# Kernel tuning notes

Hardware: AMD Instinct MI355X
Metric: run time of the kernel (lower is better)

Reference implementation:

```python
import jax, jax.numpy as jnp
import numpy as np

H = 16  # n_heads

def setup_inputs() -> dict:
    key = jax.random.key(0)
    ks = jax.random.split(key, 12)
    B, L, S, D = 4, 2048, 2048, 1024
    E = D // H  # d_keys = d_values = 64
    s = 1.0 / np.sqrt(D)
    inp = {
        "queries": jax.random.normal(ks[0], (B, L, D), jnp.float32),
        "keys": jax.random.normal(ks[1], (B, S, D), jnp.float32),
        "values": jax.random.normal(ks[2], (B, S, D), jnp.float32),
        # causal boolean mask: True = masked out
        "attn_mask": jnp.triu(jnp.ones((L, S), jnp.bool_), k=1)[None, None],
        "Wq": jax.random.normal(ks[3], (H * E, D), jnp.float32) * s,
        "bq": jnp.zeros((H * E,), jnp.float32),
        "Wk": jax.random.normal(ks[4], (H * E, D), jnp.float32) * s,
        "bk": jnp.zeros((H * E,), jnp.float32),
        "Wv": jax.random.normal(ks[5], (H * E, D), jnp.float32) * s,
        "bv": jnp.zeros((H * E,), jnp.float32),
        "Wo": jax.random.normal(ks[6], (D, H * E), jnp.float32) * s,
        "bo": jnp.zeros((D,), jnp.float32),
    }
    return inp


def reference(queries, keys, values, attn_mask, Wq, bq, Wk, bk, Wv, bv, Wo, bo):
    B, L, D = queries.shape
    S = keys.shape[1]
    E = Wq.shape[0] // H
    # QKV projections + head split: (B, L/S, H, E)
    q = (queries @ Wq.T + bq).reshape(B, L, H, E)
    k = (keys @ Wk.T + bk).reshape(B, S, H, E)
    v = (values @ Wv.T + bv).reshape(B, S, H, E)
    scale = 1.0 / jnp.sqrt(jnp.asarray(E, q.dtype))
    scores = jnp.einsum("blhe,bshe->bhls", q, k) * scale  # (B,H,L,S)
    scores = jnp.where(attn_mask, jnp.asarray(-jnp.inf, scores.dtype), scores)
    A = jax.nn.softmax(scores, axis=-1)
    out = jnp.einsum("bhls,bshe->blhe", A, v).reshape(B, L, H * E)
    return out @ Wo.T + bo
```

## Files before the change

kernel.cpp:

```cpp
#include <hip/hip_runtime.h>
#include <hip/hip_bf16.h>

typedef float f32x4 __attribute__((ext_vector_type(4)));
typedef short s16x8 __attribute__((ext_vector_type(8)));
typedef short s16x4 __attribute__((ext_vector_type(4)));
typedef unsigned short u16;

#define H_ 16
#define E_ 64
#define D_ 1024
#define L_ 2048
#define NQT 32
#define SCL2E 0.18033688011f

__device__ __forceinline__ u16 f2bf(float f) {
  union { float f; unsigned u; } v; v.f = f;
  unsigned u = v.u;
  u += 0x7fffu + ((u >> 16) & 1u);
  return (u16)(u >> 16);
}

__device__ __forceinline__ unsigned pkbf(float a, float b) {
  unsigned r;
  asm("v_cvt_pk_bf16_f32 %0, %1, %2" : "=v"(r) : "v"(a), "v"(b));
  return r;
}

__device__ __forceinline__ void gld16(const u16* g, u16* l) {
  __builtin_amdgcn_global_load_lds((const __attribute__((address_space(1))) void*)g,
                                   (__attribute__((address_space(3))) void*)l, 16, 0, 0);
}

__global__ __launch_bounds__(256) void cvtall(const float* __restrict__ q,
                                              const float* __restrict__ k,
                                              const float* __restrict__ v,
                                              const float* __restrict__ w0,
                                              const float* __restrict__ w1,
                                              const float* __restrict__ w2,
                                              const float* __restrict__ w3,
                                              u16* __restrict__ qd,
                                              u16* __restrict__ kd,
                                              u16* __restrict__ vd,
                                              u16* __restrict__ d0,
                                              u16* __restrict__ d1,
                                              u16* __restrict__ d2,
                                              u16* __restrict__ d3) {
  const int b = blockIdx.x;
  const float* src; u16* dst; float s = 1.0f; size_t off;
  if (b < 12288) {
    const int y = b >> 12, bx = b & 4095;
    src = y == 0 ? q : (y == 1 ? k : v);
    dst = y == 0 ? qd : (y == 1 ? kd : vd);
    off = ((size_t)bx * 256 + threadIdx.x) * 8;
  } else {
    const int b2 = b - 12288, y = b2 >> 9, bx = b2 & 511;
    src = y == 0 ? w0 : (y == 1 ? w1 : (y == 2 ? w2 : w3));
    dst = y == 0 ? d0 : (y == 1 ? d1 : (y == 2 ? d2 : d3));
    if (y == 0) s = SCL2E;
    off = ((size_t)bx * 256 + threadIdx.x) * 8;
  }
  const f32x4 a = *(const f32x4*)(src + off);
  const f32x4 c = *(const f32x4*)(src + off + 4);
  s16x8 r;
#pragma unroll
  for (int j = 0; j < 4; ++j) { r[j] = (short)f2bf(a[j] * s); r[j + 4] = (short)f2bf(c[j] * s); }
  *(s16x8*)(dst + off) = r;
}

template<int PERMUTE>
__global__ __launch_bounds__(256) void gemm_lds(const u16* __restrict__ A,
                                                const u16* __restrict__ W,
                                                const float* __restrict__ bias,
                                                void* __restrict__ outp,
                                                int M, int N, int K, float bsc)
{
  __shared__ __align__(16) u16 As[2][128][64];
  __shared__ __align__(16) u16 Bs[2][128][64];
  const int tid = threadIdx.x;
  const int m0 = blockIdx.y * 128, n0 = blockIdx.x * 128;
  const int w = tid >> 6, lane = tid & 63, g = lane >> 4, li = lane & 15;
  const int wr = w >> 1, wc = w & 1;

  int sOff[4];
#pragma unroll
  for (int j = 0; j < 4; ++j) {
    const int s = (w * 4 + j) * 64 + lane;
    const int row = s >> 3, c8 = s & 7;
    sOff[j] = row * K + ((c8 ^ (row & 7)) * 8);
  }

  f32x4 acc[4][4];
#pragma unroll
  for (int i = 0; i < 4; ++i)
#pragma unroll
    for (int j = 0; j < 4; ++j) acc[i][j] = (f32x4){0.f, 0.f, 0.f, 0.f};

  const u16* Abase = A + (size_t)m0 * K;
  const u16* Wbase = W + (size_t)n0 * K;
  const int swz = li & 7;

  auto STAGE = [&](int k0, int bf) {
#pragma unroll
    for (int j = 0; j < 4; ++j) {
      gld16(Abase + k0 + sOff[j], &As[bf][(w * 4 + j) * 8][0]);
      gld16(Wbase + k0 + sOff[j], &Bs[bf][(w * 4 + j) * 8][0]);
    }
  };

  STAGE(0, 0);
  __syncthreads();
  int buf = 0;
  for (int k0 = 0; k0 < K; k0 += 64) {
    if (k0 + 64 < K) STAGE(k0 + 64, buf ^ 1);

    s16x8 a[2][4], b[2][4];
#pragma unroll
    for (int kk = 0; kk < 2; ++kk) {
      const int cg = ((kk * 4 + g) ^ swz) * 8;
#pragma unroll
      for (int mi = 0; mi < 4; ++mi) a[kk][mi] = *(const s16x8*)&As[buf][wr * 64 + mi * 16 + li][cg];
#pragma unroll
      for (int ni = 0; ni < 4; ++ni) b[kk][ni] = *(const s16x8*)&Bs[buf][wc * 64 + ni * 16 + li][cg];
    }
#pragma unroll
    for (int kk = 0; kk < 2; ++kk)
#pragma unroll
      for (int mi = 0; mi < 4; ++mi)
#pragma unroll
        for (int ni = 0; ni < 4; ++ni)
          acc[mi][ni] = __builtin_amdgcn_mfma_f32_16x16x32_bf16(a[kk][mi], b[kk][ni], acc[mi][ni], 0, 0, 0);

    __syncthreads();
    buf ^= 1;
  }

#pragma unroll
  for (int mi = 0; mi < 4; ++mi) {
#pragma unroll
    for (int ni = 0; ni < 4; ++ni) {
      const int row = m0 + wr * 64 + mi * 16 + g * 4;
      const int col = n0 + wc * 64 + ni * 16 + li;
      const float bv = bias[col] * bsc;
      if (PERMUTE == 2) {
        s16x4 pk;
#pragma unroll
        for (int r = 0; r < 4; ++r) pk[r] = (short)f2bf(acc[mi][ni][r] + bv);
        const int bb = row >> 11, lq = row & (L_ - 1);
        const int hh = col >> 6, e = col & (E_ - 1);
        *(s16x4*)&((u16*)outp)[(((size_t)bb * H_ + hh) * E_ + e) * L_ + lq] = pk;
      } else {
#pragma unroll
        for (int r = 0; r < 4; ++r) {
          const float v = acc[mi][ni][r] + bv;
          const int rr = row + r;
          if (PERMUTE == 1) {
            const int bb = rr >> 11, lq = rr & (L_ - 1);
            const int hh = col >> 6, e = col & (E_ - 1);
            ((u16*)outp)[(((size_t)bb * H_ + hh) * L_ + lq) * E_ + e] = f2bf(v);
          } else {
            ((float*)outp)[(size_t)rr * N + col] = v;
          }
        }
      }
    }
  }
}

template<int A_BF16, int PERMUTE>
__global__ __launch_bounds__(256) void gemm_bt(const void* __restrict__ Aptr,
                                               const float* __restrict__ W,
                                               const float* __restrict__ bias,
                                               void* __restrict__ outp,
                                               int M, int N, int K, float osc)
{
  __shared__ __align__(16) short As[2][128][40];
  __shared__ __align__(16) short Bs[2][128][40];
  const int tid = threadIdx.x;
  const int m0 = blockIdx.y * 128, n0 = blockIdx.x * 128;
  const int w = tid >> 6, lane = tid & 63, g = lane >> 4, li = lane & 15;
  const int wr = w >> 1, wc = w & 1;

  f32x4 acc[4][4];
#pragma unroll
  for (int i = 0; i < 4; ++i)
#pragma unroll
    for (int j = 0; j < 4; ++j) acc[i][j] = (f32x4){0.f, 0.f, 0.f, 0.f};

  f32x4 ra0[2], ra1[2];
  s16x8 rab[2];
  f32x4 rb0[2], rb1[2];

  auto LOAD = [&](int k0) {
#pragma unroll
    for (int p = 0; p < 2; ++p) {
      const int c = p * 256 + tid, row = c >> 2, kc = (c & 3) * 8;
      if (A_BF16) {
        rab[p] = *(const s16x8*)((const u16*)Aptr + (size_t)(m0 + row) * K + k0 + kc);
      } else {
        const float* ap = (const float*)Aptr + (size_t)(m0 + row) * K + k0 + kc;
        ra0[p] = *(const f32x4*)ap; ra1[p] = *(const f32x4*)(ap + 4);
      }
      const float* wp = W + (size_t)(n0 + row) * K + k0 + kc;
      rb0[p] = *(const f32x4*)wp; rb1[p] = *(const f32x4*)(wp + 4);
    }
  };
  auto WRITE = [&](int buf) {
#pragma unroll
    for (int p = 0; p < 2; ++p) {
      const int c = p * 256 + tid, row = c >> 2, kc = (c & 3) * 8;
      if (A_BF16) {
        *(s16x8*)&As[buf][row][kc] = rab[p];
      } else {
        s16x8 r;
#pragma unroll
        for (int j = 0; j < 4; ++j) { r[j] = (short)f2bf(ra0[p][j]); r[j + 4] = (short)f2bf(ra1[p][j]); }
        *(s16x8*)&As[buf][row][kc] = r;
      }
      s16x8 rb;
#pragma unroll
      for (int j = 0; j < 4; ++j) { rb[j] = (short)f2bf(rb0[p][j]); rb[j + 4] = (short)f2bf(rb1[p][j]); }
      *(s16x8*)&Bs[buf][row][kc] = rb;
    }
  };

  LOAD(0); WRITE(0);
  __syncthreads();
  int cur = 0;
  for (int k0 = 0; k0 < K; k0 += 32) {
    const bool more = (k0 + 32 < K);
    if (more) LOAD(k0 + 32);

    s16x8 a[4], b[4];
#pragma unroll
    for (int mi = 0; mi < 4; ++mi) a[mi] = *(const s16x8*)&As[cur][wr * 64 + mi * 16 + li][g * 8];
#pragma unroll
    for (int ni = 0; ni < 4; ++ni) b[ni] = *(const s16x8*)&Bs[cur][wc * 64 + ni * 16 + li][g * 8];
#pragma unroll
    for (int mi = 0; mi < 4; ++mi)
#pragma unroll
      for (int ni = 0; ni < 4; ++ni)
        acc[mi][ni] = __builtin_amdgcn_mfma_f32_16x16x32_bf16(a[mi], b[ni], acc[mi][ni], 0, 0, 0);

    if (more) { WRITE(cur ^ 1); __syncthreads(); }
    cur ^= 1;
  }

#pragma unroll
  for (int mi = 0; mi < 4; ++mi) {
#pragma unroll
    for (int ni = 0; ni < 4; ++ni) {
      const int row = m0 + wr * 64 + mi * 16 + g * 4;
      const int col = n0 + wc * 64 + ni * 16 + li;
      const float bv = bias[col];
      if (PERMUTE == 2) {
        s16x4 pk;
#pragma unroll
        for (int r = 0; r < 4; ++r) pk[r] = (short)f2bf((acc[mi][ni][r] + bv) * osc);
        const int bb = row >> 11, lq = row & (L_ - 1);
        const int hh = col >> 6, e = col & (E_ - 1);
        *(s16x4*)&((u16*)outp)[(((size_t)bb * H_ + hh) * E_ + e) * L_ + lq] = pk;
      } else {
#pragma unroll
        for (int r = 0; r < 4; ++r) {
          const float v = (acc[mi][ni][r] + bv) * osc;
          const int rr = row + r;
          if (PERMUTE == 1) {
            const int bb = rr >> 11, lq = rr & (L_ - 1);
            const int hh = col >> 6, e = col & (E_ - 1);
            ((u16*)outp)[(((size_t)bb * H_ + hh) * L_ + lq) * E_ + e] = f2bf(v);
          } else {
            ((float*)outp)[(size_t)rr * N + col] = v;
          }
        }
      }
    }
  }
}

__global__ __launch_bounds__(256) void attn_kernel(const u16* __restrict__ qp,
                                                   const u16* __restrict__ kp,
                                                   const u16* __restrict__ vtp,
                                                   u16* __restrict__ op)
{
  __shared__ __align__(16) u16 Ks[2][4096];
  __shared__ __align__(16) u16 Vs[2][4096];
  const int tid = threadIdx.x;
  const unsigned wgid = blockIdx.x;
  const int bh = (wgid & 7) * 8 + ((wgid >> 3) & 7);
  const int qx = wgid >> 6;
  const int w = tid >> 6, lane = tid & 63, g = lane >> 4, li = lane & 15;
  const size_t base  = (size_t)bh * L_ * E_;
  const size_t baseT = (size_t)bh * E_ * L_;
  const int bb = bh >> 4, hh = bh & 15;

  const int qbA = NQT - 1 - qx;
  const int qbB = qx;
  const int qbaseA = qbA * 64, qbaseB = qbB * 64;

  const u16* qrA = qp + base + (size_t)(qbaseA + w * 16 + li) * E_;
  const s16x8 qa0A = *(const s16x8*)(qrA + g * 8);
  const s16x8 qa1A = *(const s16x8*)(qrA + 32 + g * 8);
  const u16* qrB = qp + base + (size_t)(qbaseB + w * 16 + li) * E_;
  const s16x8 qa0B = *(const s16x8*)(qrB + g * 8);
  const s16x8 qa1B = *(const s16x8*)(qrB + 32 + g * 8);

  f32x4 oA[4], oB[4];
  float mA = -1e30f, lA = 0.f, mB = -1e30f, lB = 0.f;
#pragma unroll
  for (int nc = 0; nc < 4; ++nc) { oA[nc] = (f32x4){0.f,0.f,0.f,0.f}; oB[nc] = (f32x4){0.f,0.f,0.f,0.f}; }

  int kSrc[2], vSrc[2];
#pragma unroll
  for (int j = 0; j < 2; ++j) {
    const int s = (w * 2 + j) * 64 + lane;
    const int row = s >> 3;
    const int c8 = (s & 7) ^ ((row & 3) | (((row >> 3) & 1) << 2));
    kSrc[j] = row * E_ + c8 * 8;
    vSrc[j] = row * L_ + c8 * 8;
  }
  auto stage = [&](int t, int buf) {
    const int kvb = t * 64;
#pragma unroll
    for (int j = 0; j < 2; ++j) {
      gld16(kp + base + (size_t)kvb * E_ + kSrc[j], &Ks[buf][(w * 2 + j) * 512]);
      gld16(vtp + baseT + kvb + vSrc[j],            &Vs[buf][(w * 2 + j) * 512]);
    }
  };

  const int swzk = li & 7;
  const int swzv = (li & 3) | (((li >> 3) & 1) << 2);
  int kRd[8], vRd[8];
#pragma unroll
  for (int inst = 0; inst < 4; ++inst) {
    const int bs = (32 * (inst >> 1) + 4 * (inst & 1) + 8 * (li >> 2) + (li & 3)) * 8;
    kRd[inst * 2]     = (bs + (g ^ swzk)) * 8;
    kRd[inst * 2 + 1] = (bs + ((g + 4) ^ swzk)) * 8;
  }
#pragma unroll
  for (int nc = 0; nc < 4; ++nc) {
    const int es = (nc * 16 + li) * 8;
    vRd[nc * 2]     = (es + (g ^ swzv)) * 8;
    vRd[nc * 2 + 1] = (es + ((g + 4) ^ swzv)) * 8;
  }

  auto qk = [&](const s16x8* kf, const s16x8& q0, const s16x8& q1, f32x4* p,
                int t, int qb, int qbase) {
#pragma unroll
    for (int inst = 0; inst < 4; ++inst) {
      f32x4 sf = (f32x4){0.f, 0.f, 0.f, 0.f};
      sf = __builtin_amdgcn_mfma_f32_16x16x32_bf16(kf[inst * 2],     q0, sf, 0, 0, 0);
      sf = __builtin_amdgcn_mfma_f32_16x16x32_bf16(kf[inst * 2 + 1], q1, sf, 0, 0, 0);
      p[inst] = sf;
    }
    if (t == qb) {
      const int qrow = qbase + w * 16 + li;
      const int kvb = t * 64;
#pragma unroll
      for (int inst = 0; inst < 4; ++inst)
#pragma unroll
        for (int r = 0; r < 4; ++r)
          if (kvb + 32 * (inst >> 1) + 8 * g + 4 * (inst & 1) + r > qrow) p[inst][r] = -1e30f;
    }
  };
  auto sm = [&](f32x4* p, float& m_run, float& l_run, f32x4* o, unsigned* pk) -> float {
    float m0_ = fmaxf(fmaxf(p[0][0], p[0][1]), fmaxf(p[0][2], p[0][3]));
    float m1_ = fmaxf(fmaxf(p[1][0], p[1][1]), fmaxf(p[1][2], p[1][3]));
    float m2_ = fmaxf(fmaxf(p[2][0], p[2][1]), fmaxf(p[2][2], p[2][3]));
    float m3_ = fmaxf(fmaxf(p[3][0], p[3][1]), fmaxf(p[3][2], p[3][3]));
    const float mx16 = fmaxf(fmaxf(m0_, m1_), fmaxf(m2_, m3_));
    if (__any(mx16 > m_run + 8.0f)) {
      float mx = fmaxf(mx16, __shfl_xor(mx16, 16));
      mx = fmaxf(mx, __shfl_xor(mx, 32));
      const float mn = fmaxf(m_run, mx);
      const float alpha = __builtin_amdgcn_exp2f(m_run - mn);
      m_run = mn;
      l_run *= alpha;
#pragma unroll
      for (int nc = 0; nc < 4; ++nc)
#pragma unroll
        for (int r = 0; r < 4; ++r) o[nc][r] *= alpha;
    }
    float rs = 0.f;
#pragma unroll
    for (int inst = 0; inst < 4; ++inst) {
      const float e0 = __builtin_amdgcn_exp2f(p[inst][0] - m_run);
      const float e1 = __builtin_amdgcn_exp2f(p[inst][1] - m_run);
      const float e2 = __builtin_amdgcn_exp2f(p[inst][2] - m_run);
      const float e3 = __builtin_amdgcn_exp2f(p[inst][3] - m_run);
      rs += (e0 + e1) + (e2 + e3);
      pk[inst * 2]     = pkbf(e0, e1);
      pk[inst * 2 + 1] = pkbf(e2, e3);
    }
    return rs;
  };
  auto pv = [&](const s16x8* vf, const unsigned* pk, f32x4* o) {
    union { s16x8 v; unsigned u[4]; } A0, A1;
    A0.u[0] = pk[0]; A0.u[1] = pk[1]; A0.u[2] = pk[2]; A0.u[3] = pk[3];
    A1.u[0] = pk[4]; A1.u[1] = pk[5]; A1.u[2] = pk[6]; A1.u[3] = pk[7];
#pragma unroll
    for (int nc = 0; nc < 4; ++nc) {
      o[nc] = __builtin_amdgcn_mfma_f32_16x16x32_bf16(vf[nc * 2],     A0.v, o[nc], 0, 0, 0);
      o[nc] = __builtin_amdgcn_mfma_f32_16x16x32_bf16(vf[nc * 2 + 1], A1.v, o[nc], 0, 0, 0);
    }
  };

  stage(0, 0);
  __syncthreads();
  int buf = 0;
  unsigned pkA[8], pkB[8];
  for (int t = 0; t <= qbA; ++t) {
    const bool more = (t < qbA);
    const bool doB  = (t <= qbB);
    if (more) stage(t + 1, buf ^ 1);

    s16x8 kf[8];
#pragma unroll
    for (int i = 0; i < 8; ++i) kf[i] = *(const s16x8*)&Ks[buf][kRd[i]];
    f32x4 pA[4], pB[4];
    qk(kf, qa0A, qa1A, pA, t, qbA, qbaseA);
    if (doB) qk(kf, qa0B, qa1B, pB, t, qbB, qbaseB);

    s16x8 vf[8];
#pragma unroll
    for (int i = 0; i < 8; ++i) vf[i] = *(const s16x8*)&Vs[buf][vRd[i]];

    float rsA = sm(pA, mA, lA, oA, pkA);
    float rsB = 0.f;
    if (doB) rsB = sm(pB, mB, lB, oB, pkB);

    pv(vf, pkA, oA);
    if (doB) pv(vf, pkB, oB);

    rsA += __shfl_xor(rsA, 16); rsA += __shfl_xor(rsA, 32);
    lA += rsA;
    if (doB) { rsB += __shfl_xor(rsB, 16); rsB += __shfl_xor(rsB, 32); lB += rsB; }

    if (more) __syncthreads();
    buf ^= 1;
  }

  auto epilogue = [&](const f32x4* o, float l_run, int qbase) {
    const float inv = 1.0f / l_run;
    u16* orow = op + ((size_t)bb * L_ + qbase + w * 16 + li) * D_ + hh * E_;
#pragma unroll
    for (int nc = 0; nc < 4; ++nc) {
      union { s16x4 v; unsigned u[2]; } P;
      P.u[0] = pkbf(o[nc][0] * inv, o[nc][1] * inv);
      P.u[1] = pkbf(o[nc][2] * inv, o[nc][3] * inv);
      *(s16x4*)&orow[nc * 16 + g * 4] = P.v;
    }
  };
  epilogue(oA, lA, qbaseA);
  epilogue(oB, lB, qbaseB);
}

extern "C" void kernel_launch(void* const* d_in, const int* in_sizes, int n_in,
                              void* d_out, int out_size, void* d_ws, size_t ws_size,
                              hipStream_t stream) {
  const float* queries = (const float*)d_in[0];
  const float* keys    = (const float*)d_in[1];
  const float* values  = (const float*)d_in[2];
  const float* Wq = (const float*)d_in[4];
  const float* bq = (const float*)d_in[5];
  const float* Wk = (const float*)d_in[6];
  const float* bk = (const float*)d_in[7];
  const float* Wv = (const float*)d_in[8];
  const float* bv = (const float*)d_in[9];
  const float* Wo = (const float*)d_in[10];
  const float* bo = (const float*)d_in[11];

  const size_t MD = (size_t)8192 * 1024;
  const size_t WN = (size_t)1024 * 1024;
  u16* qbuf = (u16*)d_ws;
  u16* kbuf = qbuf + MD;
  u16* vbuf = kbuf + MD;
  u16* abuf = vbuf + MD;

  dim3 blk(256);
  dim3 ggrid(8, 64);

  const size_t need = (4 * MD + 4 * WN) * sizeof(u16);
  if (ws_size >= need) {
    u16* qcv = abuf;
    u16* kcv = qbuf;
    u16* vcv = kbuf;
    u16* wqb = abuf + MD;
    u16* wkb = wqb + WN;
    u16* wvb = wkb + WN;
    u16* wob = wvb + WN;

    cvtall<<<dim3(14336), blk, 0, stream>>>(queries, keys, values, Wq, Wk, Wv, Wo,
                                            qcv, kcv, vcv, wqb, wkb, wvb, wob);

    gemm_lds<2><<<ggrid, blk, 0, stream>>>(vcv, wvb, bv, vbuf, 8192, 1024, 1024, 1.0f);
    gemm_lds<1><<<ggrid, blk, 0, stream>>>(kcv, wkb, bk, kbuf, 8192, 1024, 1024, 1.0f);
    gemm_lds<1><<<ggrid, blk, 0, stream>>>(qcv, wqb, bq, qbuf, 8192, 1024, 1024, SCL2E);
    attn_kernel<<<dim3(1024), blk, 0, stream>>>(qbuf, kbuf, vbuf, abuf);
    gemm_lds<0><<<ggrid, blk, 0, stream>>>(abuf, wob, bo, d_out, 8192, 1024, 1024, 1.0f);
  } else {
    gemm_bt<0, 1><<<ggrid, blk, 0, stream>>>(queries, Wq, bq, qbuf, 8192, 1024, 1024, SCL2E);
    gemm_bt<0, 1><<<ggrid, blk, 0, stream>>>(keys,    Wk, bk, kbuf, 8192, 1024, 1024, 1.0f);
    gemm_bt<0, 2><<<ggrid, blk, 0, stream>>>(values,  Wv, bv, vbuf, 8192, 1024, 1024, 1.0f);
    attn_kernel<<<dim3(1024), blk, 0, stream>>>(qbuf, kbuf, vbuf, abuf);
    gemm_bt<1, 0><<<ggrid, blk, 0, stream>>>(abuf, Wo, bo, d_out, 8192, 1024, 1024, 1.0f);
  }
}
```

Before: 203.1 us.

## Split paired causal query tiles into separate workgroups and defer row-sum reduction

The attention kernel used to pair a long and a short causal query tile in one workgroup so that K/V tiles loaded once were shared by both. It now launches one workgroup per query tile (2048 instead of 1024), ordered longest first, which gives more parallelism and fewer live registers per thread. The per-iteration cross-lane shuffle reduction of the softmax row sum is moved to a single reduction after the loop. In exchange, K/V loads are no longer shared between two tiles, so LDS and global traffic rise, and load balance now relies on the scheduler picking up the descending-length work.

```diff
diff --git a/kernel.cpp b/kernel.cpp
--- a/kernel.cpp
+++ b/kernel.cpp
@@ -287,27 +287,21 @@
   const int tid = threadIdx.x;
   const unsigned wgid = blockIdx.x;
   const int bh = (wgid & 7) * 8 + ((wgid >> 3) & 7);
-  const int qx = wgid >> 6;
+  const int qb = NQT - 1 - (int)(wgid >> 6);
   const int w = tid >> 6, lane = tid & 63, g = lane >> 4, li = lane & 15;
   const size_t base  = (size_t)bh * L_ * E_;
   const size_t baseT = (size_t)bh * E_ * L_;
   const int bb = bh >> 4, hh = bh & 15;
-
-  const int qbA = NQT - 1 - qx;
-  const int qbB = qx;
-  const int qbaseA = qbA * 64, qbaseB = qbB * 64;
-
-  const u16* qrA = qp + base + (size_t)(qbaseA + w * 16 + li) * E_;
-  const s16x8 qa0A = *(const s16x8*)(qrA + g * 8);
-  const s16x8 qa1A = *(const s16x8*)(qrA + 32 + g * 8);
-  const u16* qrB = qp + base + (size_t)(qbaseB + w * 16 + li) * E_;
-  const s16x8 qa0B = *(const s16x8*)(qrB + g * 8);
-  const s16x8 qa1B = *(const s16x8*)(qrB + 32 + g * 8);
-
-  f32x4 oA[4], oB[4];
-  float mA = -1e30f, lA = 0.f, mB = -1e30f, lB = 0.f;
-#pragma unroll
-  for (int nc = 0; nc < 4; ++nc) { oA[nc] = (f32x4){0.f,0.f,0.f,0.f}; oB[nc] = (f32x4){0.f,0.f,0.f,0.f}; }
+  const int qbase = qb * 64;
+
+  const u16* qr = qp + base + (size_t)(qbase + w * 16 + li) * E_;
+  const s16x8 qa0 = *(const s16x8*)(qr + g * 8);
+  const s16x8 qa1 = *(const s16x8*)(qr + 32 + g * 8);
+
+  f32x4 o[4];
+  float m_run = -1e30f, l_run = 0.f;
+#pragma unroll
+  for (int nc = 0; nc < 4; ++nc) o[nc] = (f32x4){0.f, 0.f, 0.f, 0.f};
 
   int kSrc[2], vSrc[2];
 #pragma unroll
@@ -343,13 +337,22 @@
     vRd[nc * 2 + 1] = (es + ((g + 4) ^ swzv)) * 8;
   }
 
-  auto qk = [&](const s16x8* kf, const s16x8& q0, const s16x8& q1, f32x4* p,
-                int t, int qb, int qbase) {
+  stage(0, 0);
+  __syncthreads();
+  int buf = 0;
+  for (int t = 0; t <= qb; ++t) {
+    const bool more = (t < qb);
+    if (more) stage(t + 1, buf ^ 1);
+
+    s16x8 kf[8];
+#pragma unroll
+    for (int i = 0; i < 8; ++i) kf[i] = *(const s16x8*)&Ks[buf][kRd[i]];
+    f32x4 p[4];
 #pragma unroll
     for (int inst = 0; inst < 4; ++inst) {
       f32x4 sf = (f32x4){0.f, 0.f, 0.f, 0.f};
-      sf = __builtin_amdgcn_mfma_f32_16x16x32_bf16(kf[inst * 2],     q0, sf, 0, 0, 0);
-      sf = __builtin_amdgcn_mfma_f32_16x16x32_bf16(kf[inst * 2 + 1], q1, sf, 0, 0, 0);
+      sf = __builtin_amdgcn_mfma_f32_16x16x32_bf16(kf[inst * 2],     qa0, sf, 0, 0, 0);
+      sf = __builtin_amdgcn_mfma_f32_16x16x32_bf16(kf[inst * 2 + 1], qa1, sf, 0, 0, 0);
       p[inst] = sf;
     }
     if (t == qb) {
@@ -361,25 +364,31 @@
         for (int r = 0; r < 4; ++r)
           if (kvb + 32 * (inst >> 1) + 8 * g + 4 * (inst & 1) + r > qrow) p[inst][r] = -1e30f;
     }
-  };
-  auto sm = [&](f32x4* p, float& m_run, float& l_run, f32x4* o, unsigned* pk) -> float {
-    float m0_ = fmaxf(fmaxf(p[0][0], p[0][1]), fmaxf(p[0][2], p[0][3]));
-    float m1_ = fmaxf(fmaxf(p[1][0], p[1][1]), fmaxf(p[1][2], p[1][3]));
-    float m2_ = fmaxf(fmaxf(p[2][0], p[2][1]), fmaxf(p[2][2], p[2][3]));
-    float m3_ = fmaxf(fmaxf(p[3][0], p[3][1]), fmaxf(p[3][2], p[3][3]));
-    const float mx16 = fmaxf(fmaxf(m0_, m1_), fmaxf(m2_, m3_));
-    if (__any(mx16 > m_run + 8.0f)) {
-      float mx = fmaxf(mx16, __shfl_xor(mx16, 16));
-      mx = fmaxf(mx, __shfl_xor(mx, 32));
-      const float mn = fmaxf(m_run, mx);
-      const float alpha = __builtin_amdgcn_exp2f(m_run - mn);
-      m_run = mn;
-      l_run *= alpha;
-#pragma unroll
-      for (int nc = 0; nc < 4; ++nc)
-#pragma unroll
-        for (int r = 0; r < 4; ++r) o[nc][r] *= alpha;
-    }
+
+    s16x8 vf[8];
+#pragma unroll
+    for (int i = 0; i < 8; ++i) vf[i] = *(const s16x8*)&Vs[buf][vRd[i]];
+
+    {
+      float m0_ = fmaxf(fmaxf(p[0][0], p[0][1]), fmaxf(p[0][2], p[0][3]));
+      float m1_ = fmaxf(fmaxf(p[1][0], p[1][1]), fmaxf(p[1][2], p[1][3]));
+      float m2_ = fmaxf(fmaxf(p[2][0], p[2][1]), fmaxf(p[2][2], p[2][3]));
+      float m3_ = fmaxf(fmaxf(p[3][0], p[3][1]), fmaxf(p[3][2], p[3][3]));
+      const float mx16 = fmaxf(fmaxf(m0_, m1_), fmaxf(m2_, m3_));
+      if (__any(mx16 > m_run + 8.0f)) {
+        float mx = fmaxf(mx16, __shfl_xor(mx16, 16));
+        mx = fmaxf(mx, __shfl_xor(mx, 32));
+        const float mn = fmaxf(m_run, mx);
+        const float alpha = __builtin_amdgcn_exp2f(m_run - mn);
+        m_run = mn;
+        l_run *= alpha;
+#pragma unroll
+        for (int nc = 0; nc < 4; ++nc)
+#pragma unroll
+          for (int r = 0; r < 4; ++r) o[nc][r] *= alpha;
+      }
+    }
+    unsigned pk[8];
     float rs = 0.f;
 #pragma unroll
     for (int inst = 0; inst < 4; ++inst) {
@@ -391,9 +400,8 @@
       pk[inst * 2]     = pkbf(e0, e1);
       pk[inst * 2 + 1] = pkbf(e2, e3);
     }
-    return rs;
-  };
-  auto pv = [&](const s16x8* vf, const unsigned* pk, f32x4* o) {
+    l_run += rs;
+
     union { s16x8 v; unsigned u[4]; } A0, A1;
     A0.u[0] = pk[0]; A0.u[1] = pk[1]; A0.u[2] = pk[2]; A0.u[3] = pk[3];
     A1.u[0] = pk[4]; A1.u[1] = pk[5]; A1.u[2] = pk[6]; A1.u[3] = pk[7];
@@ -402,56 +410,23 @@
       o[nc] = __builtin_amdgcn_mfma_f32_16x16x32_bf16(vf[nc * 2],     A0.v, o[nc], 0, 0, 0);
       o[nc] = __builtin_amdgcn_mfma_f32_16x16x32_bf16(vf[nc * 2 + 1], A1.v, o[nc], 0, 0, 0);
     }
-  };
-
-  stage(0, 0);
-  __syncthreads();
-  int buf = 0;
-  unsigned pkA[8], pkB[8];
-  for (int t = 0; t <= qbA; ++t) {
-    const bool more = (t < qbA);
-    const bool doB  = (t <= qbB);
-    if (more) stage(t + 1, buf ^ 1);
-
-    s16x8 kf[8];
-#pragma unroll
-    for (int i = 0; i < 8; ++i) kf[i] = *(const s16x8*)&Ks[buf][kRd[i]];
-    f32x4 pA[4], pB[4];
-    qk(kf, qa0A, qa1A, pA, t, qbA, qbaseA);
-    if (doB) qk(kf, qa0B, qa1B, pB, t, qbB, qbaseB);
-
-    s16x8 vf[8];
-#pragma unroll
-    for (int i = 0; i < 8; ++i) vf[i] = *(const s16x8*)&Vs[buf][vRd[i]];
-
-    float rsA = sm(pA, mA, lA, oA, pkA);
-    float rsB = 0.f;
-    if (doB) rsB = sm(pB, mB, lB, oB, pkB);
-
-    pv(vf, pkA, oA);
-    if (doB) pv(vf, pkB, oB);
-
-    rsA += __shfl_xor(rsA, 16); rsA += __shfl_xor(rsA, 32);
-    lA += rsA;
-    if (doB) { rsB += __shfl_xor(rsB, 16); rsB += __shfl_xor(rsB, 32); lB += rsB; }
 
     if (more) __syncthreads();
     buf ^= 1;
   }
 
-  auto epilogue = [&](const f32x4* o, float l_run, int qbase) {
-    const float inv = 1.0f / l_run;
-    u16* orow = op + ((size_t)bb * L_ + qbase + w * 16 + li) * D_ + hh * E_;
-#pragma unroll
-    for (int nc = 0; nc < 4; ++nc) {
-      union { s16x4 v; unsigned u[2]; } P;
-      P.u[0] = pkbf(o[nc][0] * inv, o[nc][1] * inv);
-      P.u[1] = pkbf(o[nc][2] * inv, o[nc][3] * inv);
-      *(s16x4*)&orow[nc * 16 + g * 4] = P.v;
-    }
-  };
-  epilogue(oA, lA, qbaseA);
-  epilogue(oB, lB, qbaseB);
+  float lsum = l_run;
+  lsum += __shfl_xor(lsum, 16);
+  lsum += __shfl_xor(lsum, 32);
+  const float inv = 1.0f / lsum;
+  u16* orow = op + ((size_t)bb * L_ + qbase + w * 16 + li) * D_ + hh * E_;
+#pragma unroll
+  for (int nc = 0; nc < 4; ++nc) {
+    union { s16x4 v; unsigned u[2]; } P;
+    P.u[0] = pkbf(o[nc][0] * inv, o[nc][1] * inv);
+    P.u[1] = pkbf(o[nc][2] * inv, o[nc][3] * inv);
+    *(s16x4*)&orow[nc * 16 + g * 4] = P.v;
+  }
 }
 
 extern "C" void kernel_launch(void* const* d_in, const int* in_sizes, int n_in,
@@ -495,13 +470,13 @@
     gemm_lds<2><<<ggrid, blk, 0, stream>>>(vcv, wvb, bv, vbuf, 8192, 1024, 1024, 1.0f);
     gemm_lds<1><<<ggrid, blk, 0, stream>>>(kcv, wkb, bk, kbuf, 8192, 1024, 1024, 1.0f);
     gemm_lds<1><<<ggrid, blk, 0, stream>>>(qcv, wqb, bq, qbuf, 8192, 1024, 1024, SCL2E);
-    attn_kernel<<<dim3(1024), blk, 0, stream>>>(qbuf, kbuf, vbuf, abuf);
+    attn_kernel<<<dim3(2048), blk, 0, stream>>>(qbuf, kbuf, vbuf, abuf);
     gemm_lds<0><<<ggrid, blk, 0, stream>>>(abuf, wob, bo, d_out, 8192, 1024, 1024, 1.0f);
   } else {
     gemm_bt<0, 1><<<ggrid, blk, 0, stream>>>(queries, Wq, bq, qbuf, 8192, 1024, 1024, SCL2E);
     gemm_bt<0, 1><<<ggrid, blk, 0, stream>>>(keys,    Wk, bk, kbuf, 8192, 1024, 1024, 1.0f);
     gemm_bt<0, 2><<<ggrid, blk, 0, stream>>>(values,  Wv, bv, vbuf, 8192, 1024, 1024, 1.0f);
-    attn_kernel<<<dim3(1024), blk, 0, stream>>>(qbuf, kbuf, vbuf, abuf);
+    attn_kernel<<<dim3(2048), blk, 0, stream>>>(qbuf, kbuf, vbuf, abuf);
     gemm_bt<1, 0><<<ggrid, blk, 0, stream>>>(abuf, Wo, bo, d_out, 8192, 1024, 1024, 1.0f);
   }
 }
```

Result: faster. 186.5 us (-8.2%).
